# Kernel optimization log

Measured on AMD Instinct MI355X. Metric: run time of the kernel, lower is better.

Reference implementation:

```python
import jax, jax.numpy as jnp
import numpy as np

B, A = 64, 32            # graphs, atoms per graph
N, E = B * A, B * A * A  # nodes, fully-connected edges (incl. self-loops)
H, LAT = 512, 256        # hidden_dim, latent_dim
L = 4                    # num CSP layers
NF = 10                  # sinusoid frequencies -> dis_dim = 2*NF*3 = 60
MAXA = 100
DIS = 2 * NF * 3
EIN = 2 * H + 9 + DIS    # edge_mlp input width = 1093


def _lin(k, fan_in, shape):
    return jax.random.normal(k, shape, jnp.float32) * (1.0 / np.sqrt(fan_in))


def setup_inputs() -> dict:
    key = jax.random.key(0)
    ks = jax.random.split(key, 20)
    t = jax.random.normal(ks[0], (B, LAT), jnp.float32)
    atom_types = jax.random.randint(ks[1], (N,), 1, MAXA + 1, dtype=jnp.int32)
    frac_coords = jax.random.uniform(ks[2], (N, 3), jnp.float32)
    lattices = jax.random.normal(ks[3], (B, 3, 3), jnp.float32)
    node2graph = jnp.repeat(jnp.arange(B, dtype=jnp.int32), A)
    # fc edges per graph, row-major like dense_to_sparse(block_diag(ones))
    base = (np.arange(B, dtype=np.int64) * A)[:, None]
    ii = np.repeat(np.arange(A), A)
    jj = np.tile(np.arange(A), A)
    src = (base + ii[None, :]).reshape(-1)
    dst = (base + jj[None, :]).reshape(-1)
    edge_index = jnp.asarray(np.stack([src, dst]), dtype=jnp.int32)
    params = dict(
        emb_table=jax.random.normal(ks[4], (MAXA, H), jnp.float32),
        W_latent=_lin(ks[5], H + LAT, (H + LAT, H)), b_latent=jnp.zeros((H,), jnp.float32),
        edge_W1=_lin(ks[6], EIN, (L, EIN, H)), edge_b1=jnp.zeros((L, H), jnp.float32),
        edge_W2=_lin(ks[7], H, (L, H, H)), edge_b2=jnp.zeros((L, H), jnp.float32),
        node_W1=_lin(ks[8], 2 * H, (L, 2 * H, H)), node_b1=jnp.zeros((L, H), jnp.float32),
        node_W2=_lin(ks[9], H, (L, H, H)), node_b2=jnp.zeros((L, H), jnp.float32),
        coord_W=_lin(ks[10], H, (H, 3)),
        lattice_W=_lin(ks[11], H, (H, 9)),
    )
    return dict(t=t, frac_coords=frac_coords, lattices=lattices, **params,
                atom_types=atom_types, node2graph=node2graph, edge_index=edge_index)


def reference(t, frac_coords, lattices, emb_table, W_latent, b_latent,
              edge_W1, edge_b1, edge_W2, edge_b2,
              node_W1, node_b1, node_W2, node_b2,
              coord_W, lattice_W, atom_types, node2graph, edge_index):
    silu = jax.nn.silu
    src, dst = edge_index[0], edge_index[1]
    edge2graph = node2graph[src]
    # gen_edges (fc): frac_diff per edge
    frac_diff = (frac_coords[dst] - frac_coords[src]) % 1.0            # [E,3]
    # SinusoidsEmbedding (same for every layer)
    freqs = 2.0 * jnp.pi * jnp.arange(NF, dtype=jnp.float32)
    fd = (frac_diff[:, :, None] * freqs).reshape(-1, 3 * NF)
    fd_emb = jnp.concatenate([jnp.sin(fd), jnp.cos(fd)], axis=-1)      # [E,60]
    # lattice inner products (ip=True), broadcast to edges
    lat_ip = jnp.einsum('bij,bkj->bik', lattices, lattices).reshape(-1, 9)
    lat_e = lat_ip[edge2graph]                                          # [E,9]
    # node embedding + time conditioning
    nf = emb_table[atom_types - 1]                                      # [N,H]
    nf = jnp.concatenate([nf, t[node2graph]], axis=1) @ W_latent + b_latent
    ones_e = jnp.ones((src.shape[0], 1), nf.dtype)
    for i in range(L):
        hi, hj = nf[src], nf[dst]
        ein = jnp.concatenate([hi, hj, lat_e, fd_emb], axis=1)          # [E,1093]
        ef = silu(silu(ein @ edge_W1[i] + edge_b1[i]) @ edge_W2[i] + edge_b2[i])
        agg = jax.ops.segment_sum(ef, src, num_segments=N)
        deg = jax.ops.segment_sum(ones_e, src, num_segments=N)
        agg = agg / jnp.maximum(deg, 1.0)                               # scatter-mean
        nin = jnp.concatenate([nf, agg], axis=1)                        # [N,2H]
        nf = nf + silu(silu(nin @ node_W1[i] + node_b1[i]) @ node_W2[i] + node_b2[i])
    coord_out = nf @ coord_W                                            # [N,3]
    gf = jax.ops.segment_sum(nf, node2graph, num_segments=B) / A        # graph mean
    lattice_out = (gf @ lattice_W).reshape(-1, 3, 3)
    lattice_out = jnp.einsum('bij,bjk->bik', lattice_out, lattices)     # ip=True
    return (lattice_out, coord_out)
```

## Files before the change

kernel.cpp:

```cpp
#include <hip/hip_runtime.h>
#include <math.h>


typedef short bf16x8 __attribute__((ext_vector_type(8)));
typedef float f32x4 __attribute__((ext_vector_type(4)));

__device__ __forceinline__ float silu_f(float x) {
    float e = __builtin_amdgcn_exp2f(x * -1.44269504088896f);
    return x * __builtin_amdgcn_rcpf(1.0f + e);
}
__device__ __forceinline__ unsigned short f2bf(float x) {
    unsigned int u = __float_as_uint(x);
    u += 0x7fffu + ((u >> 16) & 1u);
    return (unsigned short)(u >> 16);
}
__device__ __forceinline__ unsigned int cvt_pk_bf16(float lo, float hi) {
    unsigned int r;
    asm("v_cvt_pk_bf16_f32 %0, %1, %2" : "=v"(r) : "v"(lo), "v"(hi));
    return r;
}

#define NF_OFF    0
#define UAGG_OFF  (2048*512)
#define VT_OFF    (2*2048*512)
#define H1_OFF    (VT_OFF + 524288)
#define WBF_OFF   (H1_OFF + 524288)
#define SZ_INITT (512*768)
#define SZ_UVT   (1024*512)
#define SZ_W1DT  (512*64)
#define SZ_W2T   (512*512)
#define SZ_NW1T  (512*1024)
#define SZ_NW2T  (512*512)
#define SZ_LAYER (SZ_UVT+SZ_W1DT+SZ_W2T+SZ_NW1T+SZ_NW2T)

__global__ __launch_bounds__(256) void k_prep(
    const float* __restrict__ Wl, const float* __restrict__ eW1,
    const float* __restrict__ eW2, const float* __restrict__ nW1,
    const float* __restrict__ nW2, unsigned short* __restrict__ wbf)
{
    __shared__ float tile[32][33];
    int bid = blockIdx.x;
    const float* src; int K; unsigned short* dst; int t;
    if (bid < 384) { src = Wl; K = 768; dst = wbf; t = bid; }
    else {
        int b = bid - 384; int l = b / 1568; int j = b - l * 1568;
        const float* e1 = eW1 + (size_t)l * 1093 * 512;
        unsigned short* base = wbf + SZ_INITT + (size_t)l * SZ_LAYER;
        if (j < 256)      { src = e1;                       K = 512;  dst = base;                                   t = j; }
        else if (j < 512) { src = e1 + 512*512;             K = 512;  dst = base + 512*512;                         t = j-256; }
        else if (j < 544) { src = e1 + 1033*512;            K = 60;   dst = base + SZ_UVT;                          t = j-512; }
        else if (j < 800) { src = eW2 + (size_t)l*512*512;  K = 512;  dst = base + SZ_UVT+SZ_W1DT;                  t = j-544; }
        else if (j <1312) { src = nW1 + (size_t)l*1024*512; K = 1024; dst = base + SZ_UVT+SZ_W1DT+SZ_W2T;           t = j-800; }
        else              { src = nW2 + (size_t)l*512*512;  K = 512;  dst = base + SZ_UVT+SZ_W1DT+SZ_W2T+SZ_NW1T;   t = j-1312; }
    }
    int tr = t >> 4, tc = t & 15;
    int k0 = tr * 32, nn0 = tc * 32;
    {
        int r8 = threadIdx.x >> 5, cc = threadIdx.x & 31;
        #pragma unroll
        for (int rr = 0; rr < 4; ++rr) {
            int row = rr*8 + r8;
            int k = k0 + row;
            tile[row][cc] = (k < K) ? src[(size_t)k*512 + nn0 + cc] : 0.f;
        }
    }
    __syncthreads();
    int nt_loc = threadIdx.x >> 7;
    int l = (threadIdx.x >> 1) & 63;
    int jh = threadIdx.x & 1;
    int lj = l & 15, lh = l >> 4;
    float v0 = tile[lh*8 + jh*4 + 0][nt_loc*16 + lj];
    float v1 = tile[lh*8 + jh*4 + 1][nt_loc*16 + lj];
    float v2 = tile[lh*8 + jh*4 + 2][nt_loc*16 + lj];
    float v3 = tile[lh*8 + jh*4 + 3][nt_loc*16 + lj];
    uint2 pk = { cvt_pk_bf16(v0, v1), cvt_pk_bf16(v2, v3) };
    *(uint2*)&dst[((size_t)(tr*32 + tc*2 + nt_loc)*64 + l)*8 + jh*4] = pk;
}

__global__ __launch_bounds__(256) void k_init(
    const float* __restrict__ tvec, const float* __restrict__ emb,
    const unsigned short* __restrict__ WT, const float* __restrict__ bl,
    const int* __restrict__ atom_types, float* __restrict__ nf)
{
    __shared__ __align__(16) unsigned short cat_s[16*768];
    int n0 = (blockIdx.x >> 1) * 16, half = blockIdx.x & 1, tid = threadIdx.x;
    for (int idx = tid; idx < 16*192; idx += 256) {
        int m = idx / 192, q = idx - m * 192;
        int k4 = q * 4, n = n0 + m;
        float4 v;
        if (k4 < 512) v = *(const float4*)&emb[(size_t)(atom_types[n]-1)*512 + k4];
        else          v = *(const float4*)&tvec[(size_t)(n>>5)*256 + (k4-512)];
        uint2 pk = { cvt_pk_bf16(v.x, v.y), cvt_pk_bf16(v.z, v.w) };
        *(uint2*)&cat_s[m*768 + (k4 ^ ((m&7)<<3))] = pk;
    }
    __syncthreads();
    int w = tid >> 6, l = tid & 63, lj = l & 15, lh = l >> 4;
    f32x4 acc[4];
    #pragma unroll
    for (int nt = 0; nt < 4; ++nt) acc[nt] = (f32x4){0.f,0.f,0.f,0.f};
    for (int kt = 0; kt < 24; ++kt) {
        int k = kt*32 + lh*8;
        bf16x8 a = *(const bf16x8*)&cat_s[lj*768 + (k ^ ((lj&7)<<3))];
        #pragma unroll
        for (int nt = 0; nt < 4; ++nt) {
            bf16x8 b = *(const bf16x8*)&WT[(((size_t)kt*32 + half*16 + w*4 + nt)*64 + l)*8];
            acc[nt] = __builtin_amdgcn_mfma_f32_16x16x32_bf16(a, b, acc[nt], 0, 0, 0);
        }
    }
    #pragma unroll
    for (int nt = 0; nt < 4; ++nt) {
        int c = half*256 + w*64 + nt*16 + lj;
        float bv = bl[c];
        #pragma unroll
        for (int r = 0; r < 4; ++r)
            nf[(size_t)(n0 + lh*4 + r)*512 + c] = acc[nt][r] + bv;
    }
}

__global__ __launch_bounds__(256) void k_uv(
    const float* __restrict__ nf, const unsigned short* __restrict__ WT,
    const float* __restrict__ lat, const float* __restrict__ W1c,
    const float* __restrict__ b1, float* __restrict__ Up,
    unsigned short* __restrict__ VT)
{
    __shared__ __align__(16) unsigned short a_s[16*512];
    int n0 = (blockIdx.x >> 1) * 16, half = blockIdx.x & 1;
    int g = n0 >> 5, j0 = n0 & 31, tid = threadIdx.x;
    for (int idx = tid; idx < 16*128; idx += 256) {
        int m = idx >> 7, q = idx & 127;
        int k4 = q * 4;
        float4 v = *(const float4*)&nf[(size_t)(n0+m)*512 + k4];
        uint2 pk = { cvt_pk_bf16(v.x, v.y), cvt_pk_bf16(v.z, v.w) };
        *(uint2*)&a_s[m*512 + (k4 ^ ((m&7)<<3))] = pk;
    }
    __syncthreads();
    int w = tid >> 6, l = tid & 63, lj = l & 15, lh = l >> 4;
    const unsigned short* Wh = WT + (size_t)half*512*512;
    f32x4 acc[8];
    #pragma unroll
    for (int nt = 0; nt < 8; ++nt) acc[nt] = (f32x4){0.f,0.f,0.f,0.f};
    for (int kt = 0; kt < 16; ++kt) {
        int k = kt*32 + lh*8;
        bf16x8 a = *(const bf16x8*)&a_s[lj*512 + (k ^ ((lj&7)<<3))];
        #pragma unroll
        for (int nt = 0; nt < 8; ++nt) {
            bf16x8 b = *(const bf16x8*)&Wh[(((size_t)kt*32 + w*8 + nt)*64 + l)*8];
            acc[nt] = __builtin_amdgcn_mfma_f32_16x16x32_bf16(a, b, acc[nt], 0, 0, 0);
        }
    }
    if (half == 0) {
        float L[9], lip[9];
        #pragma unroll
        for (int i = 0; i < 9; ++i) L[i] = lat[g*9 + i];
        #pragma unroll
        for (int i = 0; i < 3; ++i)
            #pragma unroll
            for (int kk = 0; kk < 3; ++kk)
                lip[i*3+kk] = L[i*3]*L[kk*3] + L[i*3+1]*L[kk*3+1] + L[i*3+2]*L[kk*3+2];
        #pragma unroll
        for (int nt = 0; nt < 8; ++nt) {
            int c = w*128 + nt*16 + lj;
            float p3 = b1[c];
            #pragma unroll
            for (int t9 = 0; t9 < 9; ++t9) p3 += lip[t9] * W1c[t9*512 + c];
            #pragma unroll
            for (int r = 0; r < 4; ++r)
                Up[(size_t)(n0 + lh*4 + r)*512 + c] = acc[nt][r] + p3;
        }
    } else {
        int l2 = lj + 16*((j0 + lh*4) >> 3);
        int off8 = (lh*4) & 7;
        #pragma unroll
        for (int nt = 0; nt < 8; ++nt) {
            int ct = w*8 + nt;
            uint2 pk = { cvt_pk_bf16(acc[nt][0], acc[nt][1]),
                         cvt_pk_bf16(acc[nt][2], acc[nt][3]) };
            *(uint2*)&VT[(size_t)g*16384 + (size_t)ct*512 + l2*8 + off8] = pk;
        }
    }
}

__global__ __launch_bounds__(512) void k_edge(
    const float* __restrict__ Up, const unsigned short* __restrict__ VT,
    const float* __restrict__ frac,
    const unsigned short* __restrict__ W1dT,
    const unsigned short* __restrict__ W2T, const float* __restrict__ b2,
    float* __restrict__ agg)
{
    __shared__ __align__(16) unsigned short ef1_s[64*512];
    int n0 = blockIdx.x * 2, g = n0 >> 5, tid = threadIdx.x;
    int wid = tid >> 6, l = tid & 63, lj = l & 15, lh = l >> 4;
    const unsigned short* VTg = VT + (size_t)g*16384;

    {
        float di[2][2][3];
        #pragma unroll
        for (int h = 0; h < 2; ++h)
            #pragma unroll
            for (int dd = 0; dd < 2; ++dd) {
                int dstn = g*32 + dd*16 + lj;
                #pragma unroll
                for (int comp = 0; comp < 3; ++comp) {
                    float d = frac[dstn*3 + comp] - frac[(n0+h)*3 + comp];
                    d -= floorf(d);
                    di[h][dd][comp] = d;
                }
            }
        bf16x8 fdf[2][4];
        #pragma unroll
        for (int kt = 0; kt < 2; ++kt)
            #pragma unroll
            for (int mt = 0; mt < 4; ++mt) {
                int h = mt >> 1, dd = mt & 1;
                #pragma unroll
                for (int kk = 0; kk < 8; ++kk) {
                    int k = kt*32 + lh*8 + kk;
                    float val = 0.f;
                    if (k < 60) {
                        int isCos = k >= 30;
                        int dq = k - (isCos ? 30 : 0);
                        int comp = dq >= 20 ? 2 : (dq >= 10 ? 1 : 0);
                        int f = dq - comp*10;
                        float u = di[h][dd][comp] * (float)f;
                        u -= floorf(u);
                        val = isCos ? __builtin_amdgcn_cosf(u) : __builtin_amdgcn_sinf(u);
                    }
                    fdf[kt][mt][kk] = (short)f2bf(val);
                }
            }
        bf16x8 ind[2];
        #pragma unroll
        for (int dd = 0; dd < 2; ++dd)
            #pragma unroll
            for (int kk = 0; kk < 8; ++kk)
                ind[dd][kk] = (short)((lh*8 + kk == dd*16 + lj) ? 0x3F80 : 0);

        #pragma unroll
        for (int q = 0; q < 4; ++q) {
            int ct = wid*4 + q;
            f32x4 a1[4];
            #pragma unroll
            for (int mt = 0; mt < 4; ++mt) a1[mt] = (f32x4){0.f,0.f,0.f,0.f};
            bf16x8 vf = *(const bf16x8*)&VTg[((size_t)ct*64 + l)*8];
            #pragma unroll
            for (int mt = 0; mt < 4; ++mt)
                a1[mt] = __builtin_amdgcn_mfma_f32_16x16x32_bf16(vf, ind[mt&1], a1[mt], 0, 0, 0);
            #pragma unroll
            for (int kt = 0; kt < 2; ++kt) {
                bf16x8 wf = *(const bf16x8*)&W1dT[(((size_t)kt*32 + ct)*64 + l)*8];
                #pragma unroll
                for (int mt = 0; mt < 4; ++mt)
                    a1[mt] = __builtin_amdgcn_mfma_f32_16x16x32_bf16(wf, fdf[kt][mt], a1[mt], 0, 0, 0);
            }
            int c0 = wid*64 + q*16 + lh*4;
            float4 bs0 = *(const float4*)&Up[(size_t)n0*512 + c0];
            float4 bs1 = *(const float4*)&Up[(size_t)(n0+1)*512 + c0];
            #pragma unroll
            for (int mt = 0; mt < 4; ++mt) {
                float4 bb = (mt >> 1) ? bs1 : bs0;
                int m = mt*16 + lj;
                float x0 = silu_f(a1[mt][0] + bb.x);
                float x1 = silu_f(a1[mt][1] + bb.y);
                float x2 = silu_f(a1[mt][2] + bb.z);
                float x3 = silu_f(a1[mt][3] + bb.w);
                uint2 pk = { cvt_pk_bf16(x0, x1), cvt_pk_bf16(x2, x3) };
                *(uint2*)&ef1_s[m*512 + (c0 ^ ((m&7)<<3))] = pk;
            }
        }
    }
    __syncthreads();

    f32x4 acc2[4][4];
    #pragma unroll
    for (int mt = 0; mt < 4; ++mt)
        #pragma unroll
        for (int nt = 0; nt < 4; ++nt) acc2[mt][nt] = (f32x4){0.f,0.f,0.f,0.f};

    for (int kt = 0; kt < 16; ++kt) {
        int k = kt*32 + lh*8;
        bf16x8 af[4];
        #pragma unroll
        for (int mt = 0; mt < 4; ++mt) {
            int m = mt*16 + lj;
            af[mt] = *(const bf16x8*)&ef1_s[m*512 + (k ^ ((m&7)<<3))];
        }
        #pragma unroll
        for (int nt = 0; nt < 4; ++nt) {
            bf16x8 bfr = *(const bf16x8*)&W2T[(((size_t)kt*32 + wid*4 + nt)*64 + l)*8];
            #pragma unroll
            for (int mt = 0; mt < 4; ++mt)
                acc2[mt][nt] = __builtin_amdgcn_mfma_f32_16x16x32_bf16(af[mt], bfr, acc2[mt][nt], 0, 0, 0);
        }
    }

    #pragma unroll
    for (int nt = 0; nt < 4; ++nt) {
        int cc = wid*64 + nt*16 + lj;
        float bv = b2[cc];
        float s0 = 0.f, s1 = 0.f;
        #pragma unroll
        for (int mt = 0; mt < 4; ++mt)
            #pragma unroll
            for (int r = 0; r < 4; ++r) {
                float x = silu_f(acc2[mt][nt][r] + bv);
                if (mt < 2) s0 += x; else s1 += x;
            }
        s0 += __shfl_xor(s0, 16); s0 += __shfl_xor(s0, 32);
        s1 += __shfl_xor(s1, 16); s1 += __shfl_xor(s1, 32);
        if (lh == 0) {
            agg[(size_t)n0*512 + cc]     = s0 * (1.0f/32.0f);
            agg[(size_t)(n0+1)*512 + cc] = s1 * (1.0f/32.0f);
        }
    }
}

__global__ __launch_bounds__(256) void k_node1(
    const float* __restrict__ nf, const float* __restrict__ agg,
    const unsigned short* __restrict__ W1T, const float* __restrict__ b1,
    unsigned short* __restrict__ h1g)
{
    __shared__ __align__(16) unsigned short nin_s[16*1024];
    int n0 = (blockIdx.x >> 1) * 16, half = blockIdx.x & 1, tid = threadIdx.x;
    for (int idx = tid; idx < 16*256; idx += 256) {
        int m = idx >> 8, q = idx & 255;
        int k4 = q * 4;
        float4 v = (k4 < 512) ? *(const float4*)&nf[(size_t)(n0+m)*512 + k4]
                              : *(const float4*)&agg[(size_t)(n0+m)*512 + (k4-512)];
        uint2 pk = { cvt_pk_bf16(v.x, v.y), cvt_pk_bf16(v.z, v.w) };
        *(uint2*)&nin_s[m*1024 + (k4 ^ ((m&7)<<3))] = pk;
    }
    __syncthreads();
    int w = tid >> 6, l = tid & 63, lj = l & 15, lh = l >> 4;
    f32x4 acc[4];
    #pragma unroll
    for (int nt = 0; nt < 4; ++nt) acc[nt] = (f32x4){0.f,0.f,0.f,0.f};
    for (int kt = 0; kt < 32; ++kt) {
        int k = kt*32 + lh*8;
        bf16x8 a = *(const bf16x8*)&nin_s[lj*1024 + (k ^ ((lj&7)<<3))];
        #pragma unroll
        for (int nt = 0; nt < 4; ++nt) {
            bf16x8 b = *(const bf16x8*)&W1T[(((size_t)kt*32 + half*16 + w*4 + nt)*64 + l)*8];
            acc[nt] = __builtin_amdgcn_mfma_f32_16x16x32_bf16(a, b, acc[nt], 0, 0, 0);
        }
    }
    #pragma unroll
    for (int nt = 0; nt < 4; ++nt) {
        int c = half*256 + w*64 + nt*16 + lj;
        float bv = b1[c];
        #pragma unroll
        for (int r = 0; r < 4; ++r)
            h1g[(size_t)(n0 + lh*4 + r)*512 + c] = f2bf(silu_f(acc[nt][r] + bv));
    }
}

__global__ __launch_bounds__(256) void k_node2(
    float* __restrict__ nf, const unsigned short* __restrict__ h1g,
    const unsigned short* __restrict__ W2T, const float* __restrict__ b2)
{
    __shared__ __align__(16) unsigned short h1_s[16*512];
    int n0 = (blockIdx.x >> 1) * 16, half = blockIdx.x & 1, tid = threadIdx.x;
    for (int idx = tid; idx < 16*64; idx += 256) {
        int m = idx >> 6, k8 = (idx & 63) * 8;
        bf16x8 v = *(const bf16x8*)&h1g[(size_t)(n0+m)*512 + k8];
        *(bf16x8*)&h1_s[m*512 + (k8 ^ ((m&7)<<3))] = v;
    }
    __syncthreads();
    int w = tid >> 6, l = tid & 63, lj = l & 15, lh = l >> 4;
    f32x4 acc[4];
    #pragma unroll
    for (int nt = 0; nt < 4; ++nt) acc[nt] = (f32x4){0.f,0.f,0.f,0.f};
    for (int kt = 0; kt < 16; ++kt) {
        int k = kt*32 + lh*8;
        bf16x8 a = *(const bf16x8*)&h1_s[lj*512 + (k ^ ((lj&7)<<3))];
        #pragma unroll
        for (int nt = 0; nt < 4; ++nt) {
            bf16x8 b = *(const bf16x8*)&W2T[(((size_t)kt*32 + half*16 + w*4 + nt)*64 + l)*8];
            acc[nt] = __builtin_amdgcn_mfma_f32_16x16x32_bf16(a, b, acc[nt], 0, 0, 0);
        }
    }
    #pragma unroll
    for (int nt = 0; nt < 4; ++nt) {
        int c = half*256 + w*64 + nt*16 + lj;
        float bv = b2[c];
        #pragma unroll
        for (int r = 0; r < 4; ++r) {
            size_t o = (size_t)(n0 + lh*4 + r)*512 + c;
            nf[o] = nf[o] + silu_f(acc[nt][r] + bv);
        }
    }
}

__global__ __launch_bounds__(256) void k_coord(const float* __restrict__ nf,
                                               const float* __restrict__ cW,
                                               float* __restrict__ out) {
    int gid = blockIdx.x * 256 + threadIdx.x;
    if (gid >= 2048 * 3) return;
    int n = gid / 3, c = gid - n * 3;
    float s = 0.f;
    for (int k = 0; k < 512; ++k) s += nf[n * 512 + k] * cW[k * 3 + c];
    out[576 + gid] = s;
}

__global__ __launch_bounds__(256) void k_graph(const float* __restrict__ nf,
                                               const float* __restrict__ lW,
                                               const float* __restrict__ lat,
                                               float* __restrict__ out) {
    __shared__ float gf[512];
    __shared__ float lo9[9];
    int b = blockIdx.x, tid = threadIdx.x;
    float s0 = 0.f, s1 = 0.f;
    for (int r = 0; r < 32; ++r) {
        s0 += nf[(b * 32 + r) * 512 + tid];
        s1 += nf[(b * 32 + r) * 512 + tid + 256];
    }
    gf[tid]       = s0 * (1.f / 32.f);
    gf[tid + 256] = s1 * (1.f / 32.f);
    __syncthreads();
    if (tid < 9) {
        float s = 0.f;
        for (int k = 0; k < 512; ++k) s += gf[k] * lW[k * 9 + tid];
        lo9[tid] = s;
    }
    __syncthreads();
    if (tid < 9) {
        int i = tid / 3, kk = tid - (tid / 3) * 3;
        float s = lo9[i*3+0] * lat[b*9 + 0*3 + kk]
                + lo9[i*3+1] * lat[b*9 + 1*3 + kk]
                + lo9[i*3+2] * lat[b*9 + 2*3 + kk];
        out[b * 9 + tid] = s;
    }
}

extern "C" void kernel_launch(void* const* d_in, const int* in_sizes, int n_in,
                              void* d_out, int out_size, void* d_ws, size_t ws_size,
                              hipStream_t stream)
{
    const float* t    = (const float*)d_in[0];
    const float* frac = (const float*)d_in[1];
    const float* lat  = (const float*)d_in[2];
    const float* emb  = (const float*)d_in[3];
    const float* Wl   = (const float*)d_in[4];
    const float* bl   = (const float*)d_in[5];
    const float* eW1  = (const float*)d_in[6];
    const float* eb1  = (const float*)d_in[7];
    const float* eW2  = (const float*)d_in[8];
    const float* eb2  = (const float*)d_in[9];
    const float* nW1  = (const float*)d_in[10];
    const float* nb1  = (const float*)d_in[11];
    const float* nW2  = (const float*)d_in[12];
    const float* nb2  = (const float*)d_in[13];
    const float* cW   = (const float*)d_in[14];
    const float* lW   = (const float*)d_in[15];
    const int* atom_types = (const int*)d_in[16];

    float* out  = (float*)d_out;
    float* wsf  = (float*)d_ws;
    float* nf   = wsf + NF_OFF;
    float* Uagg = wsf + UAGG_OFF;
    unsigned short* VT  = (unsigned short*)(wsf + VT_OFF);
    unsigned short* h1g = (unsigned short*)(wsf + H1_OFF);
    unsigned short* wbf = (unsigned short*)(wsf + WBF_OFF);

    k_prep<<<384 + 4*1568, 256, 0, stream>>>(Wl, eW1, eW2, nW1, nW2, wbf);
    k_init<<<256, 256, 0, stream>>>(t, emb, wbf, bl, atom_types, nf);
    for (int l = 0; l < 4; ++l) {
        const unsigned short* uvT  = wbf + SZ_INITT + (size_t)l * SZ_LAYER;
        const unsigned short* w1dT = uvT + SZ_UVT;
        const unsigned short* w2T  = w1dT + SZ_W1DT;
        const unsigned short* nw1T = w2T + SZ_W2T;
        const unsigned short* nw2T = nw1T + SZ_NW1T;
        k_uv<<<256, 256, 0, stream>>>(nf, uvT, lat,
                                      eW1 + (size_t)l*1093*512 + 1024*512,
                                      eb1 + l*512, Uagg, VT);
        k_edge<<<1024, 512, 0, stream>>>(Uagg, VT, frac, w1dT, w2T,
                                         eb2 + l*512, Uagg);
        k_node1<<<256, 256, 0, stream>>>(nf, Uagg, nw1T, nb1 + l*512, h1g);
        k_node2<<<256, 256, 0, stream>>>(nf, h1g, nw2T, nb2 + l*512);
    }
    k_coord<<<24, 256, 0, stream>>>(nf, cW, out);
    k_graph<<<64, 256, 0, stream>>>(nf, lW, lat, out);
}
```

Baseline: 434.3 us.

## Precompute edge distance features once and store V in MFMA accumulator layout

The sinusoidal fractional-distance features were recomputed inside the edge kernel for every layer. They are now built once by a new k_fd kernel into a packed bf16 buffer that the edge kernel loads directly. V is stored in fp32 in the MFMA accumulator layout, so the edge kernel loads its accumulator initial values instead of running an identity-matrix MFMA. The coord kernel is also rewritten to use per-row vector loads and shuffle reductions. The cost is extra global memory traffic, since fp32 V doubles its buffer size and the feature buffer is read every layer.

```diff
diff --git a/kernel.cpp b/kernel.cpp
--- a/kernel.cpp
+++ b/kernel.cpp
@@ -22,8 +22,8 @@
 
 #define NF_OFF    0
 #define UAGG_OFF  (2048*512)
-#define VT_OFF    (2*2048*512)
-#define H1_OFF    (VT_OFF + 524288)
+#define VTD_OFF   (2*2048*512)
+#define H1_OFF    (VTD_OFF + 64*16384)
 #define WBF_OFF   (H1_OFF + 524288)
 #define SZ_INITT (512*768)
 #define SZ_UVT   (1024*512)
@@ -32,6 +32,8 @@
 #define SZ_NW1T  (512*1024)
 #define SZ_NW2T  (512*512)
 #define SZ_LAYER (SZ_UVT+SZ_W1DT+SZ_W2T+SZ_NW1T+SZ_NW2T)
+#define WBF_FLOATS ((SZ_INITT + 4*SZ_LAYER + 1)/2)
+#define FDP_OFF   (WBF_OFF + WBF_FLOATS)
 
 __global__ __launch_bounds__(256) void k_prep(
     const float* __restrict__ Wl, const float* __restrict__ eW1,
@@ -77,6 +79,56 @@
     *(uint2*)&dst[((size_t)(tr*32 + tc*2 + nt_loc)*64 + l)*8 + jh*4] = pk;
 }
 
+__global__ __launch_bounds__(64) void k_fd(const float* __restrict__ frac,
+                                           unsigned short* __restrict__ fdP)
+{
+    int bid = blockIdx.x;
+    int n0 = bid * 2, g = n0 >> 5;
+    int l = threadIdx.x, lj = l & 15, lh = l >> 4;
+    float di[2][2][3];
+    #pragma unroll
+    for (int h = 0; h < 2; ++h)
+        #pragma unroll
+        for (int dd = 0; dd < 2; ++dd) {
+            int dstn = g*32 + dd*16 + lj;
+            #pragma unroll
+            for (int comp = 0; comp < 3; ++comp) {
+                float d = frac[dstn*3 + comp] - frac[(n0+h)*3 + comp];
+                d -= floorf(d);
+                di[h][dd][comp] = d;
+            }
+        }
+    #pragma unroll
+    for (int kt = 0; kt < 2; ++kt)
+        #pragma unroll
+        for (int mt = 0; mt < 4; ++mt) {
+            int h = mt >> 1, dd = mt & 1;
+            unsigned int w[4];
+            #pragma unroll
+            for (int p = 0; p < 4; ++p) {
+                float vv[2];
+                #pragma unroll
+                for (int e = 0; e < 2; ++e) {
+                    int k = kt*32 + lh*8 + p*2 + e;
+                    float val = 0.f;
+                    if (k < 60) {
+                        int isCos = k >= 30;
+                        int dq = k - (isCos ? 30 : 0);
+                        int comp = dq >= 20 ? 2 : (dq >= 10 ? 1 : 0);
+                        int f = dq - comp*10;
+                        float u = di[h][dd][comp] * (float)f;
+                        u -= floorf(u);
+                        val = isCos ? __builtin_amdgcn_cosf(u) : __builtin_amdgcn_sinf(u);
+                    }
+                    vv[e] = val;
+                }
+                w[p] = cvt_pk_bf16(vv[0], vv[1]);
+            }
+            uint4 pk = { w[0], w[1], w[2], w[3] };
+            *(uint4*)&fdP[(((size_t)bid*8 + kt*4 + mt)*64 + l)*8] = pk;
+        }
+}
+
 __global__ __launch_bounds__(256) void k_init(
     const float* __restrict__ tvec, const float* __restrict__ emb,
     const unsigned short* __restrict__ WT, const float* __restrict__ bl,
@@ -121,11 +173,11 @@
     const float* __restrict__ nf, const unsigned short* __restrict__ WT,
     const float* __restrict__ lat, const float* __restrict__ W1c,
     const float* __restrict__ b1, float* __restrict__ Up,
-    unsigned short* __restrict__ VT)
+    float* __restrict__ VTD)
 {
     __shared__ __align__(16) unsigned short a_s[16*512];
     int n0 = (blockIdx.x >> 1) * 16, half = blockIdx.x & 1;
-    int g = n0 >> 5, j0 = n0 & 31, tid = threadIdx.x;
+    int g = n0 >> 5, tid = threadIdx.x;
     for (int idx = tid; idx < 16*128; idx += 256) {
         int m = idx >> 7, q = idx & 127;
         int k4 = q * 4;
@@ -168,21 +220,20 @@
                 Up[(size_t)(n0 + lh*4 + r)*512 + c] = acc[nt][r] + p3;
         }
     } else {
-        int l2 = lj + 16*((j0 + lh*4) >> 3);
-        int off8 = (lh*4) & 7;
+        int dd = (n0 & 31) >> 4;
         #pragma unroll
         for (int nt = 0; nt < 8; ++nt) {
             int ct = w*8 + nt;
-            uint2 pk = { cvt_pk_bf16(acc[nt][0], acc[nt][1]),
-                         cvt_pk_bf16(acc[nt][2], acc[nt][3]) };
-            *(uint2*)&VT[(size_t)g*16384 + (size_t)ct*512 + l2*8 + off8] = pk;
+            #pragma unroll
+            for (int rr = 0; rr < 4; ++rr)
+                VTD[(size_t)g*16384 + ct*512 + dd*256 + (lh*4+rr)*16 + lj] = acc[nt][rr];
         }
     }
 }
 
 __global__ __launch_bounds__(512) void k_edge(
-    const float* __restrict__ Up, const unsigned short* __restrict__ VT,
-    const float* __restrict__ frac,
+    const float* __restrict__ Up, const float* __restrict__ VTD,
+    const unsigned short* __restrict__ fdP,
     const unsigned short* __restrict__ W1dT,
     const unsigned short* __restrict__ W2T, const float* __restrict__ b2,
     float* __restrict__ agg)
@@ -190,61 +241,22 @@
     __shared__ __align__(16) unsigned short ef1_s[64*512];
     int n0 = blockIdx.x * 2, g = n0 >> 5, tid = threadIdx.x;
     int wid = tid >> 6, l = tid & 63, lj = l & 15, lh = l >> 4;
-    const unsigned short* VTg = VT + (size_t)g*16384;
 
     {
-        float di[2][2][3];
-        #pragma unroll
-        for (int h = 0; h < 2; ++h)
-            #pragma unroll
-            for (int dd = 0; dd < 2; ++dd) {
-                int dstn = g*32 + dd*16 + lj;
-                #pragma unroll
-                for (int comp = 0; comp < 3; ++comp) {
-                    float d = frac[dstn*3 + comp] - frac[(n0+h)*3 + comp];
-                    d -= floorf(d);
-                    di[h][dd][comp] = d;
-                }
-            }
         bf16x8 fdf[2][4];
         #pragma unroll
         for (int kt = 0; kt < 2; ++kt)
             #pragma unroll
-            for (int mt = 0; mt < 4; ++mt) {
-                int h = mt >> 1, dd = mt & 1;
-                #pragma unroll
-                for (int kk = 0; kk < 8; ++kk) {
-                    int k = kt*32 + lh*8 + kk;
-                    float val = 0.f;
-                    if (k < 60) {
-                        int isCos = k >= 30;
-                        int dq = k - (isCos ? 30 : 0);
-                        int comp = dq >= 20 ? 2 : (dq >= 10 ? 1 : 0);
-                        int f = dq - comp*10;
-                        float u = di[h][dd][comp] * (float)f;
-                        u -= floorf(u);
-                        val = isCos ? __builtin_amdgcn_cosf(u) : __builtin_amdgcn_sinf(u);
-                    }
-                    fdf[kt][mt][kk] = (short)f2bf(val);
-                }
-            }
-        bf16x8 ind[2];
-        #pragma unroll
-        for (int dd = 0; dd < 2; ++dd)
-            #pragma unroll
-            for (int kk = 0; kk < 8; ++kk)
-                ind[dd][kk] = (short)((lh*8 + kk == dd*16 + lj) ? 0x3F80 : 0);
+            for (int mt = 0; mt < 4; ++mt)
+                fdf[kt][mt] = *(const bf16x8*)&fdP[(((size_t)blockIdx.x*8 + kt*4 + mt)*64 + l)*8];
 
         #pragma unroll
         for (int q = 0; q < 4; ++q) {
             int ct = wid*4 + q;
             f32x4 a1[4];
             #pragma unroll
-            for (int mt = 0; mt < 4; ++mt) a1[mt] = (f32x4){0.f,0.f,0.f,0.f};
-            bf16x8 vf = *(const bf16x8*)&VTg[((size_t)ct*64 + l)*8];
-            #pragma unroll
             for (int mt = 0; mt < 4; ++mt)
-                a1[mt] = __builtin_amdgcn_mfma_f32_16x16x32_bf16(vf, ind[mt&1], a1[mt], 0, 0, 0);
+                a1[mt] = *(const f32x4*)&VTD[(size_t)g*16384 + ct*512 + (mt&1)*256 + lj*16 + lh*4];
             #pragma unroll
             for (int kt = 0; kt < 2; ++kt) {
                 bf16x8 wf = *(const bf16x8*)&W1dT[(((size_t)kt*32 + ct)*64 + l)*8];
@@ -393,12 +405,27 @@
 __global__ __launch_bounds__(256) void k_coord(const float* __restrict__ nf,
                                                const float* __restrict__ cW,
                                                float* __restrict__ out) {
-    int gid = blockIdx.x * 256 + threadIdx.x;
-    if (gid >= 2048 * 3) return;
-    int n = gid / 3, c = gid - n * 3;
-    float s = 0.f;
-    for (int k = 0; k < 512; ++k) s += nf[n * 512 + k] * cW[k * 3 + c];
-    out[576 + gid] = s;
+    int b = blockIdx.x, t = threadIdx.x;
+    int nl = t >> 3, s = t & 7;
+    int n = b*32 + nl;
+    const float* row = nf + (size_t)n*512 + s*64;
+    float p0 = 0.f, p1 = 0.f, p2 = 0.f;
+    #pragma unroll
+    for (int k4 = 0; k4 < 64; k4 += 4) {
+        float4 v = *(const float4*)&row[k4];
+        int kg = s*64 + k4;
+        p0 += v.x*cW[(kg+0)*3+0] + v.y*cW[(kg+1)*3+0] + v.z*cW[(kg+2)*3+0] + v.w*cW[(kg+3)*3+0];
+        p1 += v.x*cW[(kg+0)*3+1] + v.y*cW[(kg+1)*3+1] + v.z*cW[(kg+2)*3+1] + v.w*cW[(kg+3)*3+1];
+        p2 += v.x*cW[(kg+0)*3+2] + v.y*cW[(kg+1)*3+2] + v.z*cW[(kg+2)*3+2] + v.w*cW[(kg+3)*3+2];
+    }
+    p0 += __shfl_xor(p0, 1); p0 += __shfl_xor(p0, 2); p0 += __shfl_xor(p0, 4);
+    p1 += __shfl_xor(p1, 1); p1 += __shfl_xor(p1, 2); p1 += __shfl_xor(p1, 4);
+    p2 += __shfl_xor(p2, 1); p2 += __shfl_xor(p2, 2); p2 += __shfl_xor(p2, 4);
+    if (s == 0) {
+        out[576 + n*3 + 0] = p0;
+        out[576 + n*3 + 1] = p1;
+        out[576 + n*3 + 2] = p2;
+    }
 }
 
 __global__ __launch_bounds__(256) void k_graph(const float* __restrict__ nf,
@@ -457,11 +484,13 @@
     float* wsf  = (float*)d_ws;
     float* nf   = wsf + NF_OFF;
     float* Uagg = wsf + UAGG_OFF;
-    unsigned short* VT  = (unsigned short*)(wsf + VT_OFF);
+    float* VTD  = wsf + VTD_OFF;
     unsigned short* h1g = (unsigned short*)(wsf + H1_OFF);
     unsigned short* wbf = (unsigned short*)(wsf + WBF_OFF);
+    unsigned short* fdP = (unsigned short*)(wsf + FDP_OFF);
 
     k_prep<<<384 + 4*1568, 256, 0, stream>>>(Wl, eW1, eW2, nW1, nW2, wbf);
+    k_fd<<<1024, 64, 0, stream>>>(frac, fdP);
     k_init<<<256, 256, 0, stream>>>(t, emb, wbf, bl, atom_types, nf);
     for (int l = 0; l < 4; ++l) {
         const unsigned short* uvT  = wbf + SZ_INITT + (size_t)l * SZ_LAYER;
@@ -471,12 +500,12 @@
         const unsigned short* nw2T = nw1T + SZ_NW1T;
         k_uv<<<256, 256, 0, stream>>>(nf, uvT, lat,
                                       eW1 + (size_t)l*1093*512 + 1024*512,
-                                      eb1 + l*512, Uagg, VT);
-        k_edge<<<1024, 512, 0, stream>>>(Uagg, VT, frac, w1dT, w2T,
+                                      eb1 + l*512, Uagg, VTD);
+        k_edge<<<1024, 512, 0, stream>>>(Uagg, VTD, fdP, w1dT, w2T,
                                          eb2 + l*512, Uagg);
         k_node1<<<256, 256, 0, stream>>>(nf, Uagg, nw1T, nb1 + l*512, h1g);
         k_node2<<<256, 256, 0, stream>>>(nf, h1g, nw2T, nb2 + l*512);
     }
-    k_coord<<<24, 256, 0, stream>>>(nf, cW, out);
+    k_coord<<<64, 256, 0, stream>>>(nf, cW, out);
     k_graph<<<64, 256, 0, stream>>>(nf, lW, lat, out);
 }
```

Result: faster. 385.7 us (-11.2%).
